# Performance work log

Hardware: AMD Instinct MI355X
Metric: run time of the kernel (lower is better)

## Reference

```python
import jax, jax.numpy as jnp
import numpy as np

B, T, C = 4, 2048, 1024
H, D = 16, 64  # num_heads, head_dim; H*D == C

def setup_inputs() -> dict:
    key = jax.random.key(0)
    ks = jax.random.split(key, 5)
    s = 0.02
    return {
        "x": jax.random.normal(ks[0], (B, T, C), dtype=jnp.float32),
        "W_qkv": jax.random.normal(ks[1], (C, 3 * C), dtype=jnp.float32) * s,
        "b_qkv": jnp.zeros((3 * C,), dtype=jnp.float32),
        "W_out": jax.random.normal(ks[2], (C, C), dtype=jnp.float32) * s,
        "b_out": jnp.zeros((C,), dtype=jnp.float32),
    }

def reference(x, W_qkv, b_qkv, W_out, b_out):
    Bx, Tx, Cx = x.shape
    qkv = x @ W_qkv + b_qkv                       # [B,T,3C]
    q, k, v = jnp.split(qkv, 3, axis=-1)
    def heads(t):
        return t.reshape(Bx, Tx, H, D).transpose(0, 2, 1, 3)  # [B,H,T,D]
    q, k, v = heads(q), heads(k), heads(v)
    scale = 1.0 / jnp.sqrt(jnp.float32(D))
    attn = jnp.einsum('bhqd,bhkd->bhqk', q, k) * scale
    causal = jnp.tril(jnp.ones((Tx, Tx), dtype=bool))  # True = keep
    attn = jnp.where(causal, attn, -jnp.inf)
    attn = jax.nn.softmax(attn, axis=-1)
    out = jnp.einsum('bhqk,bhkd->bhqd', attn, v)  # [B,H,T,D]
    out = out.transpose(0, 2, 1, 3).reshape(Bx, Tx, Cx)
    return out @ W_out + b_out
```

## Files before the change

kernel.cpp:

```cpp
#include <hip/hip_runtime.h>
#include <math.h>

typedef unsigned short u16;
using bf16x8   = __attribute__((ext_vector_type(8))) __bf16;
using floatx4  = __attribute__((ext_vector_type(4))) float;
using ushortx8 = __attribute__((ext_vector_type(8))) unsigned short;
using ushortx4 = __attribute__((ext_vector_type(4))) unsigned short;
using uintx4   = __attribute__((ext_vector_type(4))) unsigned int;
using uintx2   = __attribute__((ext_vector_type(2))) unsigned int;

static __device__ __forceinline__ u16 f2bf(float f) {
  return (u16)((__float_as_uint(f) + 0x8000u) >> 16);
}
static __device__ __forceinline__ unsigned int pk2bf(float lo, float hi) {
#if __has_builtin(__builtin_amdgcn_cvt_pk_bf16_f32)
  typedef __attribute__((ext_vector_type(2))) __bf16 bf16x2_t;
  bf16x2_t r = __builtin_amdgcn_cvt_pk_bf16_f32(lo, hi);
  return *(unsigned int*)&r;
#else
  return __builtin_amdgcn_perm(__float_as_uint(hi) + 0x8000u,
                               __float_as_uint(lo) + 0x8000u, 0x07060302u);
#endif
}
static __device__ __forceinline__ float fast_exp2(float x) {
#if __has_builtin(__builtin_amdgcn_exp2f)
  return __builtin_amdgcn_exp2f(x);
#else
  return exp2f(x);
#endif
}
static __device__ __forceinline__ float fast_rcp(float x) {
#if __has_builtin(__builtin_amdgcn_rcpf)
  return __builtin_amdgcn_rcpf(x);
#else
  return 1.0f / x;
#endif
}
static __device__ __forceinline__ void gload_lds16(const void* g, void* l) {
  __builtin_amdgcn_global_load_lds(
      (const __attribute__((address_space(1))) unsigned int*)g,
      (__attribute__((address_space(3))) unsigned int*)l, 16, 0, 0);
}

static __device__ __forceinline__ void transW_tile(
    const float* __restrict__ W, u16* __restrict__ WT, int K, int N,
    int bx, int by, float (*tile)[68], int t) {
  const int kb = by * 64, nb = bx * 64;
  {
    const int kl = t >> 2, nc = (t & 3) * 16;
    const float* src = W + (size_t)(kb + kl) * N + nb + nc;
    #pragma unroll
    for (int c = 0; c < 4; c++)
      *(floatx4*)&tile[kl][nc + c * 4] = *(const floatx4*)(src + c * 4);
  }
  __syncthreads();
  {
    const int nl = t >> 2, kc = (t & 3) * 16;
    uintx4 u0, u1;
    #pragma unroll
    for (int j = 0; j < 4; j++)
      u0[j] = pk2bf(tile[kc + 2 * j][nl], tile[kc + 2 * j + 1][nl]);
    #pragma unroll
    for (int j = 0; j < 4; j++)
      u1[j] = pk2bf(tile[kc + 8 + 2 * j][nl], tile[kc + 9 + 2 * j][nl]);
    u16* dst = WT + (size_t)(nb + nl) * K + kb + kc;
    *(uintx4*)dst = u0;
    *(uintx4*)(dst + 8) = u1;
  }
}

__global__ __launch_bounds__(256) void prep(
    const float* __restrict__ x, const float* __restrict__ Wqkv,
    const float* __restrict__ Wout, u16* __restrict__ Xb,
    u16* __restrict__ WqT, u16* __restrict__ WoT) {
  __shared__ float tile[64][68];
  const int blk = blockIdx.x;
  const int t = threadIdx.x;
  if (blk < 4096) {
    const int i = (blk * 256 + t) * 8;
    floatx4 f0 = *(const floatx4*)(x + i);
    floatx4 f1 = *(const floatx4*)(x + i + 4);
    uintx4 u;
    u[0] = pk2bf(f0[0], f0[1]); u[1] = pk2bf(f0[2], f0[3]);
    u[2] = pk2bf(f1[0], f1[1]); u[3] = pk2bf(f1[2], f1[3]);
    *(uintx4*)(Xb + i) = u;
  } else if (blk < 4096 + 768) {
    const int b2 = blk - 4096;
    transW_tile(Wqkv, WqT, 1024, 3072, b2 % 48, b2 / 48, tile, t);
  } else {
    const int b3 = blk - 4096 - 768;
    transW_tile(Wout, WoT, 1024, 1024, b3 % 16, b3 / 16, tile, t);
  }
}

template <int OUT>
__global__ __launch_bounds__(256) void gemm128(
    const u16* __restrict__ A, const u16* __restrict__ Bt,
    const float* __restrict__ bias,
    u16* __restrict__ Qb, u16* __restrict__ Kb, u16* __restrict__ Vt,
    float* __restrict__ Out, int N, int K)
{
  __shared__ u16 As[128 * 64];
  __shared__ u16 Bs[128 * 64];

  const int tid  = threadIdx.x;
  const int wave = tid >> 6, lane = tid & 63;
  const int quad = lane >> 4, l15 = lane & 15;
  const int lrow = lane >> 3;
  const int scol = ((lane & 7) ^ lrow) * 8;

  const int rowBase = blockIdx.y * 128;
  const int colBase = blockIdx.x * 128;
  const int wRow = (wave >> 1) * 64;
  const int wCol = (wave & 1) * 64;

  floatx4 acc[4][4];
  #pragma unroll
  for (int i = 0; i < 4; i++)
    #pragma unroll
    for (int j = 0; j < 4; j++)
      acc[i][j] = floatx4{0.f, 0.f, 0.f, 0.f};

  const u16* Ap = A  + (size_t)(rowBase + (wave * 4) * 8 + lrow) * K + scol;
  const u16* Bp = Bt + (size_t)(colBase + (wave * 4) * 8 + lrow) * K + scol;

  for (int k0 = 0; k0 < K; k0 += 64) {
    __syncthreads();
    #pragma unroll
    for (int i = 0; i < 4; i++) {
      const int c = wave * 4 + i;
      gload_lds16(Ap + (size_t)(i * 8) * K + k0, &As[c * 512]);
      gload_lds16(Bp + (size_t)(i * 8) * K + k0, &Bs[c * 512]);
    }
    __syncthreads();

    #pragma unroll
    for (int ks = 0; ks < 2; ks++) {
      const int sw = (((ks << 2) | quad) ^ (l15 & 7)) << 3;
      bf16x8 a[4], b[4];
      #pragma unroll
      for (int mt = 0; mt < 4; mt++)
        a[mt] = *(const bf16x8*)&As[(wRow + mt * 16 + l15) * 64 + sw];
      #pragma unroll
      for (int nt = 0; nt < 4; nt++)
        b[nt] = *(const bf16x8*)&Bs[(wCol + nt * 16 + l15) * 64 + sw];
      if constexpr (OUT == 0) {
        #pragma unroll
        for (int mt = 0; mt < 4; mt++)
          #pragma unroll
          for (int nt = 0; nt < 4; nt++)
            acc[mt][nt] = __builtin_amdgcn_mfma_f32_16x16x32_bf16(a[mt], b[nt], acc[mt][nt], 0, 0, 0);
      } else {
        #pragma unroll
        for (int nt = 0; nt < 4; nt++)
          #pragma unroll
          for (int mt = 0; mt < 4; mt++)
            acc[nt][mt] = __builtin_amdgcn_mfma_f32_16x16x32_bf16(b[nt], a[mt], acc[nt][mt], 0, 0, 0);
      }
    }
  }

  if constexpr (OUT == 0) {
    const int which = colBase >> 10;
    const int cb = colBase & 1023;
    const float qscale = 0.18033688011112042f;
    #pragma unroll
    for (int mt = 0; mt < 4; mt++) {
      const int gm0 = rowBase + wRow + mt * 16 + quad * 4;
      const int bb = gm0 >> 11, t0 = gm0 & 2047;
      #pragma unroll
      for (int nt = 0; nt < 4; nt++) {
        const int gn = colBase + wCol + nt * 16 + l15;
        const int gl = cb + wCol + nt * 16 + l15;
        const float bv = bias[gn];
        const int h = gl >> 6, d = gl & 63;
        const int bh = bb * 16 + h;
        if (which == 2) {
          ushortx4 pk;
          #pragma unroll
          for (int r = 0; r < 4; r++) pk[r] = f2bf(acc[mt][nt][r] + bv);
          *(ushortx4*)&Vt[((size_t)bh * 64 + d) * 2048 + t0] = pk;
        } else if (which == 0) {
          #pragma unroll
          for (int r = 0; r < 4; r++)
            Qb[((size_t)bh * 2048 + t0 + r) * 64 + d] = f2bf((acc[mt][nt][r] + bv) * qscale);
        } else {
          #pragma unroll
          for (int r = 0; r < 4; r++)
            Kb[((size_t)bh * 2048 + t0 + r) * 64 + d] = f2bf(acc[mt][nt][r] + bv);
        }
      }
    }
  } else {
    #pragma unroll
    for (int nt = 0; nt < 4; nt++) {
      const int gn0 = colBase + wCol + nt * 16 + quad * 4;
      const floatx4 bv = *(const floatx4*)&bias[gn0];
      #pragma unroll
      for (int mt = 0; mt < 4; mt++) {
        const int gm = rowBase + wRow + mt * 16 + l15;
        floatx4 v = acc[nt][mt] + bv;
        *(floatx4*)&Out[(size_t)gm * N + gn0] = v;
      }
    }
  }
}

__global__ __launch_bounds__(256) void attn_fa(
    const u16* __restrict__ Qb, const u16* __restrict__ Kb,
    const u16* __restrict__ Vt, u16* __restrict__ Ob)
{
  __shared__ u16 Qs[128 * 64];
  __shared__ u16 Ks[2][64 * 64], Vs[2][64 * 64];

  const int tid  = threadIdx.x;
  const int wave = tid >> 6, lane = tid & 63;
  const int quad = lane >> 4, l15 = lane & 15;
  const int lrow = lane >> 3;
  const int scol = ((lane & 7) ^ lrow) * 8;

  const int bh    = blockIdx.x;
  const int qt    = 15 - (int)blockIdx.y;
  const int qbase = qt * 128;

  const u16* Qp = Qb + (size_t)bh * 2048 * 64;
  const u16* Kp = Kb + (size_t)bh * 2048 * 64;
  const u16* Vp = Vt + (size_t)bh * 64 * 2048;

  #pragma unroll
  for (int i = 0; i < 4; i++) {
    const int c = wave * 4 + i;
    gload_lds16(Qp + (size_t)(qbase + c * 8 + lrow) * 64 + scol, &Qs[c * 512]);
  }
  #pragma unroll
  for (int i = 0; i < 2; i++) {
    const int c = wave * 2 + i;
    gload_lds16(Kp + (size_t)(c * 8 + lrow) * 64 + scol, &Ks[0][c * 512]);
    gload_lds16(Vp + (size_t)(c * 8 + lrow) * 2048 + scol, &Vs[0][c * 512]);
  }
  __syncthreads();

  const int swA0 = (quad ^ (l15 & 7)) * 8;
  const int swA1 = ((4 + quad) ^ (l15 & 7)) * 8;
  bf16x8 aq[2][2];
  #pragma unroll
  for (int mt = 0; mt < 2; mt++) {
    const int row = wave * 32 + mt * 16 + l15;
    aq[mt][0] = *(const bf16x8*)&Qs[row * 64 + swA0];
    aq[mt][1] = *(const bf16x8*)&Qs[row * 64 + swA1];
  }
  __syncthreads();

  u16* Pt0 = &Qs[(wave * 2 + 0) * 1024];
  u16* Pt1 = &Qs[(wave * 2 + 1) * 1024];
  const int pwr = l15 * 64 + (quad & 1) * 4;
  const int pw_x = (quad >> 1);

  floatx4 o[2][4];
  #pragma unroll
  for (int mt = 0; mt < 2; mt++)
    #pragma unroll
    for (int dt = 0; dt < 4; dt++) o[mt][dt] = floatx4{0.f, 0.f, 0.f, 0.f};
  float lsum[2] = {0.f, 0.f};

  const int rowmax = qbase + wave * 32 + 31;
  const int nk = 2 * qt + 2;
  for (int kt = 0; kt < nk; kt++) {
    const int kbase = kt * 64;
    const int cur = kt & 1;
    if (kt + 1 < nk) {
      const int nb = kbase + 64;
      #pragma unroll
      for (int i = 0; i < 2; i++) {
        const int c = wave * 2 + i;
        gload_lds16(Kp + (size_t)(nb + c * 8 + lrow) * 64 + scol, &Ks[cur ^ 1][c * 512]);
        gload_lds16(Vp + (size_t)(c * 8 + lrow) * 2048 + nb + scol, &Vs[cur ^ 1][c * 512]);
      }
    }

    if (kbase <= rowmax) {
      bf16x8 kf[4][2];
      #pragma unroll
      for (int ct = 0; ct < 4; ct++) {
        const int row = ct * 16 + l15;
        kf[ct][0] = *(const bf16x8*)&Ks[cur][row * 64 + swA0];
        kf[ct][1] = *(const bf16x8*)&Ks[cur][row * 64 + swA1];
      }

      floatx4 st[2][4];
      #pragma unroll
      for (int mt = 0; mt < 2; mt++)
        #pragma unroll
        for (int ct = 0; ct < 4; ct++) {
          floatx4 z = floatx4{0.f, 0.f, 0.f, 0.f};
          z          = __builtin_amdgcn_mfma_f32_16x16x32_bf16(kf[ct][0], aq[mt][0], z, 0, 0, 0);
          st[mt][ct] = __builtin_amdgcn_mfma_f32_16x16x32_bf16(kf[ct][1], aq[mt][1], z, 0, 0, 0);
        }

      bf16x8 vf[4][2];
      #pragma unroll
      for (int ct = 0; ct < 4; ct++) {
        const int row = ct * 16 + l15;
        vf[ct][0] = *(const bf16x8*)&Vs[cur][row * 64 + swA0];
        vf[ct][1] = *(const bf16x8*)&Vs[cur][row * 64 + swA1];
      }

      #pragma unroll
      for (int mt = 0; mt < 2; mt++) {
        const int rowmin = qbase + wave * 32 + mt * 16;
        const bool needmask = (kbase + 63 > rowmin);
        const int qg = rowmin + l15;
        u16* Ptm = mt ? Pt1 : Pt0;
        float ls = 0.f;
        #pragma unroll
        for (int ct = 0; ct < 4; ct++) {
          float p0 = fast_exp2(st[mt][ct][0]), p1 = fast_exp2(st[mt][ct][1]);
          float p2 = fast_exp2(st[mt][ct][2]), p3 = fast_exp2(st[mt][ct][3]);
          if (needmask) {
            const int k0i = kbase + ct * 16 + quad * 4;
            if (k0i + 0 > qg) p0 = 0.f;
            if (k0i + 1 > qg) p1 = 0.f;
            if (k0i + 2 > qg) p2 = 0.f;
            if (k0i + 3 > qg) p3 = 0.f;
          }
          ls += (p0 + p1) + (p2 + p3);
          uintx2 w;
          w[0] = pk2bf(p0, p1);
          w[1] = pk2bf(p2, p3);
          const int chunk = ct * 2 + pw_x;
          *(uintx2*)&Ptm[pwr + ((chunk ^ (l15 & 7)) << 3)] = w;
        }
        lsum[mt] += ls;
      }

      #pragma unroll
      for (int mt = 0; mt < 2; mt++) {
        u16* Ptm = mt ? Pt1 : Pt0;
        const bf16x8 pb0 = *(const bf16x8*)&Ptm[l15 * 64 + swA0];
        const bf16x8 pb1 = *(const bf16x8*)&Ptm[l15 * 64 + swA1];
        #pragma unroll
        for (int dt = 0; dt < 4; dt++) {
          o[mt][dt] = __builtin_amdgcn_mfma_f32_16x16x32_bf16(vf[dt][0], pb0, o[mt][dt], 0, 0, 0);
          o[mt][dt] = __builtin_amdgcn_mfma_f32_16x16x32_bf16(vf[dt][1], pb1, o[mt][dt], 0, 0, 0);
        }
      }
    }
    __syncthreads();
  }

  const int bb = bh >> 4, h = bh & 15;
  #pragma unroll
  for (int mt = 0; mt < 2; mt++) {
    float l = lsum[mt];
    l += __shfl_xor(l, 16);
    l += __shfl_xor(l, 32);
    const float linv = fast_rcp(l);
    const int t = qbase + wave * 32 + mt * 16 + l15;
    u16* dst = Ob + ((size_t)(bb * 2048 + t)) * 1024 + h * 64 + quad * 4;
    #pragma unroll
    for (int dt = 0; dt < 4; dt++) {
      uintx2 w;
      w[0] = pk2bf(o[mt][dt][0] * linv, o[mt][dt][1] * linv);
      w[1] = pk2bf(o[mt][dt][2] * linv, o[mt][dt][3] * linv);
      *(uintx2*)(dst + dt * 16) = w;
    }
  }
}

extern "C" void kernel_launch(void* const* d_in, const int* in_sizes, int n_in,
                              void* d_out, int out_size, void* d_ws, size_t ws_size,
                              hipStream_t stream) {
  const float* x    = (const float*)d_in[0];
  const float* Wqkv = (const float*)d_in[1];
  const float* bqkv = (const float*)d_in[2];
  const float* Wout = (const float*)d_in[3];
  const float* bout = (const float*)d_in[4];

  const size_t NB = (size_t)8192 * 1024;
  u16* Xb  = (u16*)d_ws;
  u16* WqT = Xb + NB;
  u16* WoT = WqT + (size_t)3072 * 1024;
  u16* Qb  = WoT + (size_t)1024 * 1024;
  u16* Kb  = Qb + NB;
  u16* Vt  = Kb + NB;

  prep<<<5120, 256, 0, stream>>>(x, Wqkv, Wout, Xb, WqT, WoT);
  gemm128<0><<<dim3(24, 64), 256, 0, stream>>>(
      Xb, WqT, bqkv, Qb, Kb, Vt, nullptr, 3072, 1024);
  attn_fa<<<dim3(64, 16), 256, 0, stream>>>(Qb, Kb, Vt, Xb);
  gemm128<1><<<dim3(8, 64), 256, 0, stream>>>(
      Xb, WoT, bout, nullptr, nullptr, nullptr, (float*)d_out, 1024, 1024);
}
```

Before: 256.9 us.

## Pair causal query tiles per block and drop K/V double buffering

Each attention block now handles two query tiles, y and 15-y, one after the other, so every block does the same amount of causal work, and the grid is halved. K/V shared memory goes from double-buffered to single-buffered with a sync before and after each load, so loads no longer overlap compute. The P staging buffer becomes a padded per-wave 16x72 tile that is reused for each 16-row subtile. Sub-tiles lying entirely above the diagonal are now skipped. The aim is to remove tail imbalance and cut LDS use for higher occupancy, at the cost of losing the load/compute prefetch overlap.

```diff
diff --git a/kernel.cpp b/kernel.cpp
--- a/kernel.cpp
+++ b/kernel.cpp
@@ -211,7 +211,7 @@
     const u16* __restrict__ Vt, u16* __restrict__ Ob)
 {
   __shared__ u16 Qs[128 * 64];
-  __shared__ u16 Ks[2][64 * 64], Vs[2][64 * 64];
+  __shared__ u16 Ks[64 * 64], Vs[64 * 64];
 
   const int tid  = threadIdx.x;
   const int wave = tid >> 6, lane = tid & 63;
@@ -219,103 +219,91 @@
   const int lrow = lane >> 3;
   const int scol = ((lane & 7) ^ lrow) * 8;
 
-  const int bh    = blockIdx.x;
-  const int qt    = 15 - (int)blockIdx.y;
-  const int qbase = qt * 128;
+  u16* Pt = &Qs[wave * 16 * 72];
+
+  const int bh = blockIdx.x;
+  const int y  = blockIdx.y;
 
   const u16* Qp = Qb + (size_t)bh * 2048 * 64;
   const u16* Kp = Kb + (size_t)bh * 2048 * 64;
   const u16* Vp = Vt + (size_t)bh * 64 * 2048;
 
-  #pragma unroll
-  for (int i = 0; i < 4; i++) {
-    const int c = wave * 4 + i;
-    gload_lds16(Qp + (size_t)(qbase + c * 8 + lrow) * 64 + scol, &Qs[c * 512]);
-  }
-  #pragma unroll
-  for (int i = 0; i < 2; i++) {
-    const int c = wave * 2 + i;
-    gload_lds16(Kp + (size_t)(c * 8 + lrow) * 64 + scol, &Ks[0][c * 512]);
-    gload_lds16(Vp + (size_t)(c * 8 + lrow) * 2048 + scol, &Vs[0][c * 512]);
-  }
-  __syncthreads();
-
   const int swA0 = (quad ^ (l15 & 7)) * 8;
   const int swA1 = ((4 + quad) ^ (l15 & 7)) * 8;
-  bf16x8 aq[2][2];
-  #pragma unroll
-  for (int mt = 0; mt < 2; mt++) {
-    const int row = wave * 32 + mt * 16 + l15;
-    aq[mt][0] = *(const bf16x8*)&Qs[row * 64 + swA0];
-    aq[mt][1] = *(const bf16x8*)&Qs[row * 64 + swA1];
-  }
-  __syncthreads();
-
-  u16* Pt0 = &Qs[(wave * 2 + 0) * 1024];
-  u16* Pt1 = &Qs[(wave * 2 + 1) * 1024];
-  const int pwr = l15 * 64 + (quad & 1) * 4;
-  const int pw_x = (quad >> 1);
-
-  floatx4 o[2][4];
-  #pragma unroll
-  for (int mt = 0; mt < 2; mt++)
-    #pragma unroll
-    for (int dt = 0; dt < 4; dt++) o[mt][dt] = floatx4{0.f, 0.f, 0.f, 0.f};
-  float lsum[2] = {0.f, 0.f};
-
-  const int rowmax = qbase + wave * 32 + 31;
-  const int nk = 2 * qt + 2;
-  for (int kt = 0; kt < nk; kt++) {
-    const int kbase = kt * 64;
-    const int cur = kt & 1;
-    if (kt + 1 < nk) {
-      const int nb = kbase + 64;
+  const int bb = bh >> 4, h = bh & 15;
+
+  for (int ph = 0; ph < 2; ph++) {
+    const int qt = ph ? (15 - y) : y;
+    const int qbase = qt * 128;
+
+    __syncthreads();
+    #pragma unroll
+    for (int i = 0; i < 4; i++) {
+      const int c = wave * 4 + i;
+      gload_lds16(Qp + (size_t)(qbase + c * 8 + lrow) * 64 + scol, &Qs[c * 512]);
+    }
+    __syncthreads();
+
+    bf16x8 aq[2][2];
+    #pragma unroll
+    for (int mt = 0; mt < 2; mt++) {
+      const int row = wave * 32 + mt * 16 + l15;
+      aq[mt][0] = *(const bf16x8*)&Qs[row * 64 + swA0];
+      aq[mt][1] = *(const bf16x8*)&Qs[row * 64 + swA1];
+    }
+
+    floatx4 o[2][4];
+    #pragma unroll
+    for (int mt = 0; mt < 2; mt++)
+      #pragma unroll
+      for (int dt = 0; dt < 4; dt++) o[mt][dt] = floatx4{0.f, 0.f, 0.f, 0.f};
+    float lsum[2] = {0.f, 0.f};
+
+    const int rowmax = qbase + wave * 32 + 31;
+    const int nk = 2 * qt + 2;
+    for (int kt = 0; kt < nk; kt++) {
+      const int kbase = kt * 64;
+      __syncthreads();
       #pragma unroll
       for (int i = 0; i < 2; i++) {
         const int c = wave * 2 + i;
-        gload_lds16(Kp + (size_t)(nb + c * 8 + lrow) * 64 + scol, &Ks[cur ^ 1][c * 512]);
-        gload_lds16(Vp + (size_t)(c * 8 + lrow) * 2048 + nb + scol, &Vs[cur ^ 1][c * 512]);
-      }
-    }
-
-    if (kbase <= rowmax) {
-      bf16x8 kf[4][2];
+        gload_lds16(Kp + (size_t)(kbase + c * 8 + lrow) * 64 + scol, &Ks[c * 512]);
+        gload_lds16(Vp + (size_t)(c * 8 + lrow) * 2048 + kbase + scol, &Vs[c * 512]);
+      }
+      __syncthreads();
+
+      if (kbase > rowmax) continue;
+
+      bf16x8 kf[4][2], vf[4][2];
       #pragma unroll
       for (int ct = 0; ct < 4; ct++) {
         const int row = ct * 16 + l15;
-        kf[ct][0] = *(const bf16x8*)&Ks[cur][row * 64 + swA0];
-        kf[ct][1] = *(const bf16x8*)&Ks[cur][row * 64 + swA1];
-      }
-
-      floatx4 st[2][4];
-      #pragma unroll
-      for (int mt = 0; mt < 2; mt++)
+        kf[ct][0] = *(const bf16x8*)&Ks[row * 64 + swA0];
+        kf[ct][1] = *(const bf16x8*)&Ks[row * 64 + swA1];
+        vf[ct][0] = *(const bf16x8*)&Vs[row * 64 + swA0];
+        vf[ct][1] = *(const bf16x8*)&Vs[row * 64 + swA1];
+      }
+
+      #pragma unroll
+      for (int mt = 0; mt < 2; mt++) {
+        const int rowmin = qbase + wave * 32 + mt * 16;
+        if (kbase > rowmin + 15) continue;
+        const bool needmask = (kbase + 63 > rowmin);
+
+        floatx4 st[4];
         #pragma unroll
         for (int ct = 0; ct < 4; ct++) {
           floatx4 z = floatx4{0.f, 0.f, 0.f, 0.f};
-          z          = __builtin_amdgcn_mfma_f32_16x16x32_bf16(kf[ct][0], aq[mt][0], z, 0, 0, 0);
-          st[mt][ct] = __builtin_amdgcn_mfma_f32_16x16x32_bf16(kf[ct][1], aq[mt][1], z, 0, 0, 0);
+          z      = __builtin_amdgcn_mfma_f32_16x16x32_bf16(kf[ct][0], aq[mt][0], z, 0, 0, 0);
+          st[ct] = __builtin_amdgcn_mfma_f32_16x16x32_bf16(kf[ct][1], aq[mt][1], z, 0, 0, 0);
         }
 
-      bf16x8 vf[4][2];
-      #pragma unroll
-      for (int ct = 0; ct < 4; ct++) {
-        const int row = ct * 16 + l15;
-        vf[ct][0] = *(const bf16x8*)&Vs[cur][row * 64 + swA0];
-        vf[ct][1] = *(const bf16x8*)&Vs[cur][row * 64 + swA1];
-      }
-
-      #pragma unroll
-      for (int mt = 0; mt < 2; mt++) {
-        const int rowmin = qbase + wave * 32 + mt * 16;
-        const bool needmask = (kbase + 63 > rowmin);
         const int qg = rowmin + l15;
-        u16* Ptm = mt ? Pt1 : Pt0;
         float ls = 0.f;
         #pragma unroll
         for (int ct = 0; ct < 4; ct++) {
-          float p0 = fast_exp2(st[mt][ct][0]), p1 = fast_exp2(st[mt][ct][1]);
-          float p2 = fast_exp2(st[mt][ct][2]), p3 = fast_exp2(st[mt][ct][3]);
+          float p0 = fast_exp2(st[ct][0]), p1 = fast_exp2(st[ct][1]);
+          float p2 = fast_exp2(st[ct][2]), p3 = fast_exp2(st[ct][3]);
           if (needmask) {
             const int k0i = kbase + ct * 16 + quad * 4;
             if (k0i + 0 > qg) p0 = 0.f;
@@ -327,17 +315,12 @@
           uintx2 w;
           w[0] = pk2bf(p0, p1);
           w[1] = pk2bf(p2, p3);
-          const int chunk = ct * 2 + pw_x;
-          *(uintx2*)&Ptm[pwr + ((chunk ^ (l15 & 7)) << 3)] = w;
+          *(uintx2*)&Pt[l15 * 72 + ct * 16 + quad * 4] = w;
         }
         lsum[mt] += ls;
-      }
-
-      #pragma unroll
-      for (int mt = 0; mt < 2; mt++) {
-        u16* Ptm = mt ? Pt1 : Pt0;
-        const bf16x8 pb0 = *(const bf16x8*)&Ptm[l15 * 64 + swA0];
-        const bf16x8 pb1 = *(const bf16x8*)&Ptm[l15 * 64 + swA1];
+
+        const bf16x8 pb0 = *(const bf16x8*)&Pt[l15 * 72 + quad * 8];
+        const bf16x8 pb1 = *(const bf16x8*)&Pt[l15 * 72 + 32 + quad * 8];
         #pragma unroll
         for (int dt = 0; dt < 4; dt++) {
           o[mt][dt] = __builtin_amdgcn_mfma_f32_16x16x32_bf16(vf[dt][0], pb0, o[mt][dt], 0, 0, 0);
@@ -345,24 +328,22 @@
         }
       }
     }
-    __syncthreads();
-  }
-
-  const int bb = bh >> 4, h = bh & 15;
-  #pragma unroll
-  for (int mt = 0; mt < 2; mt++) {
-    float l = lsum[mt];
-    l += __shfl_xor(l, 16);
-    l += __shfl_xor(l, 32);
-    const float linv = fast_rcp(l);
-    const int t = qbase + wave * 32 + mt * 16 + l15;
-    u16* dst = Ob + ((size_t)(bb * 2048 + t)) * 1024 + h * 64 + quad * 4;
-    #pragma unroll
-    for (int dt = 0; dt < 4; dt++) {
-      uintx2 w;
-      w[0] = pk2bf(o[mt][dt][0] * linv, o[mt][dt][1] * linv);
-      w[1] = pk2bf(o[mt][dt][2] * linv, o[mt][dt][3] * linv);
-      *(uintx2*)(dst + dt * 16) = w;
+
+    #pragma unroll
+    for (int mt = 0; mt < 2; mt++) {
+      float l = lsum[mt];
+      l += __shfl_xor(l, 16);
+      l += __shfl_xor(l, 32);
+      const float linv = fast_rcp(l);
+      const int t = qbase + wave * 32 + mt * 16 + l15;
+      u16* dst = Ob + ((size_t)(bb * 2048 + t)) * 1024 + h * 64 + quad * 4;
+      #pragma unroll
+      for (int dt = 0; dt < 4; dt++) {
+        uintx2 w;
+        w[0] = pk2bf(o[mt][dt][0] * linv, o[mt][dt][1] * linv);
+        w[1] = pk2bf(o[mt][dt][2] * linv, o[mt][dt][3] * linv);
+        *(uintx2*)(dst + dt * 16) = w;
+      }
     }
   }
 }
@@ -387,7 +368,7 @@
   prep<<<5120, 256, 0, stream>>>(x, Wqkv, Wout, Xb, WqT, WoT);
   gemm128<0><<<dim3(24, 64), 256, 0, stream>>>(
       Xb, WqT, bqkv, Qb, Kb, Vt, nullptr, 3072, 1024);
-  attn_fa<<<dim3(64, 16), 256, 0, stream>>>(Qb, Kb, Vt, Xb);
+  attn_fa<<<dim3(64, 8), 256, 0, stream>>>(Qb, Kb, Vt, Xb);
   gemm128<1><<<dim3(8, 64), 256, 0, stream>>>(
       Xb, WoT, bout, nullptr, nullptr, nullptr, (float*)d_out, 1024, 1024);
 }
```

Measured after the change: 244.8 us. 1.05x faster.
